# Kernel optimization log

Hardware: AMD Instinct MI355X
Metric: run time of the kernel (lower is better)

The kernel has to match this reference:

```python
import jax, jax.numpy as jnp
import numpy as np

DIM = 1024
D_STATE = 16
D_CONV = 4
EXPAND = 2
D_INNER = EXPAND * DIM          # 2048
DT_RANK = (DIM + 15) // 16      # 64 (math.ceil(d_model/16))
BSZ = 2
SEQ = 2048


def setup_inputs() -> dict:
    key = jax.random.key(0)
    ks = jax.random.split(key, 8)
    g = lambda k, shape, scale: (jax.random.normal(k, shape, jnp.float32) * scale)
    return {
        "x": g(ks[0], (BSZ, SEQ, DIM), 1.0),
        # in_proj: Linear(d_model -> 2*d_inner, bias=False)
        "W_in": g(ks[1], (2 * D_INNER, DIM), DIM ** -0.5),
        # depthwise causal conv1d: groups=d_inner, kernel d_conv, bias=True
        "conv_w": g(ks[2], (D_INNER, 1, D_CONV), D_CONV ** -0.5),
        "conv_b": jnp.zeros((D_INNER,), jnp.float32),
        # x_proj: Linear(d_inner -> dt_rank + 2*d_state, bias=False)
        "W_xproj": g(ks[3], (DT_RANK + 2 * D_STATE, D_INNER), D_INNER ** -0.5),
        # dt_proj: Linear(dt_rank -> d_inner, bias=True)
        "W_dt": g(ks[4], (D_INNER, DT_RANK), DT_RANK ** -0.5),
        "b_dt": g(ks[5], (D_INNER,), 0.1),
        # S4D-real init: A = -exp(A_log), A_log = log(1..d_state)
        "A_log": jnp.log(jnp.broadcast_to(
            jnp.arange(1, D_STATE + 1, dtype=jnp.float32), (D_INNER, D_STATE))),
        "D": jnp.ones((D_INNER,), jnp.float32),
        # out_proj: Linear(d_inner -> d_model, bias=False)
        "W_out": g(ks[6], (DIM, D_INNER), D_INNER ** -0.5),
        # wrapper LayerNorm(dim)
        "gamma": jnp.ones((DIM,), jnp.float32),
        "beta": jnp.zeros((DIM,), jnp.float32),
    }


def reference(x, W_in, conv_w, conv_b, W_xproj, W_dt, b_dt,
              A_log, D, W_out, gamma, beta):
    B, L, _ = x.shape
    # ---- input projection, split into conv path and gate ----
    xz = x @ W_in.T                              # (B, L, 2*d_inner)
    xc, z = jnp.split(xz, 2, axis=-1)
    # ---- depthwise causal conv1d + SiLU ----
    xt = jnp.transpose(xc, (0, 2, 1))            # (B, d_inner, L)
    conv = jax.lax.conv_general_dilated(
        xt, conv_w, window_strides=(1,), padding=[(D_CONV - 1, 0)],
        dimension_numbers=("NCH", "OIH", "NCH"), feature_group_count=D_INNER)
    u = jax.nn.silu(jnp.transpose(conv + conv_b[None, :, None], (0, 2, 1)))  # (B,L,d_inner)
    # ---- input-dependent delta, B, C ----
    xdbc = u @ W_xproj.T                          # (B, L, dt_rank + 2*d_state)
    dt = xdbc[..., :DT_RANK]
    Bm = xdbc[..., DT_RANK:DT_RANK + D_STATE]     # (B, L, d_state)
    Cm = xdbc[..., DT_RANK + D_STATE:]            # (B, L, d_state)
    delta = jax.nn.softplus(dt @ W_dt.T + b_dt)   # (B, L, d_inner)
    A = -jnp.exp(A_log)                           # (d_inner, d_state)
    # ---- selective scan: h_t = exp(dt*A) h_{t-1} + dt*B_t*u_t ; y_t = <h_t, C_t> ----
    def step(h, inputs):
        d_t, u_t, B_t, C_t = inputs               # (B,d_inner),(B,d_inner),(B,S),(B,S)
        dA = jnp.exp(d_t[:, :, None] * A)         # (B, d_inner, S)
        h = h * dA + (d_t * u_t)[:, :, None] * B_t[:, None, :]
        y = jnp.einsum("bds,bs->bd", h, C_t)
        return h, y
    tm = lambda a: jnp.transpose(a, (1, 0, 2))    # time-major for scan
    h0 = jnp.zeros((B, D_INNER, D_STATE), x.dtype)
    _, ys = jax.lax.scan(step, h0, (tm(delta), tm(u), tm(Bm), tm(Cm)))
    y = jnp.transpose(ys, (1, 0, 2)) + u * D      # skip term D*u
    y = y * jax.nn.silu(z)                        # gate
    out = y @ W_out.T                             # (B, L, dim)
    # ---- wrapper LayerNorm(dim), eps=1e-5 ----
    mean = out.mean(-1, keepdims=True)
    var = out.var(-1, keepdims=True)
    return (out - mean) * jax.lax.rsqrt(var + 1e-5) * gamma + beta
```

## Files before the change

### kernel.cpp

```cpp
#include <hip/hip_runtime.h>
#include <stdint.h>

typedef unsigned short u16;
typedef __bf16 bf16x8 __attribute__((ext_vector_type(8)));
typedef unsigned short u16x8 __attribute__((ext_vector_type(8)));
typedef unsigned short u16x4 __attribute__((ext_vector_type(4)));
typedef float f32x4 __attribute__((ext_vector_type(4)));

#define BSZ 2
#define SEQ 2048
#define DIM 1024
#define D_INNER 2048
#define DT_RANK 64
#define D_STATE 16
#define XPROJ_N 96
#define NCHUNK 32
#define CHUNK_T 64
#define LOG2E 1.44269504f

#define N_X   4194304
#define N_W   4194304
#define N_WX  196608
#define N_WDT 131072
#define N_WO  2097152
#define N_XD  393216

__device__ __forceinline__ float bf2f(u16 h) {
    return __uint_as_float(((unsigned)h) << 16);
}
__device__ __forceinline__ u16 f2bf(float f) {
    unsigned u = __float_as_uint(f);
    unsigned r = (u + 0x7FFFu + ((u >> 16) & 1u)) >> 16;
    return (u16)r;
}

__device__ __forceinline__ f32x4 mfma16(bf16x8 a, bf16x8 b, f32x4 c) {
    return __builtin_amdgcn_mfma_f32_16x16x32_bf16(a, b, c, 0, 0, 0);
}

__device__ __forceinline__ void gload_lds16(const void* g, void* l) {
    __builtin_amdgcn_global_load_lds(
        (const __attribute__((address_space(1))) unsigned int*)(uintptr_t)g,
        (__attribute__((address_space(3))) unsigned int*)(uintptr_t)l,
        16, 0, 0);
}

__device__ __forceinline__ void split4(const float* __restrict__ in,
                                       u16* __restrict__ hi, u16* __restrict__ lo,
                                       long i)
{
    f32x4 v = *(const f32x4*)(in + i);
    u16x4 h, l;
    #pragma unroll
    for (int j = 0; j < 4; j++) {
        u16 hh = f2bf(v[j]);
        h[j] = hh;
        l[j] = f2bf(v[j] - bf2f(hh));
    }
    *(u16x4*)(hi + i) = h;
    *(u16x4*)(lo + i) = l;
}

__global__ __launch_bounds__(256)
void megasplit4(const float* __restrict__ x,  u16* __restrict__ xh,  u16* __restrict__ xl,
                const float* __restrict__ w,  u16* __restrict__ wh,  u16* __restrict__ wl,
                const float* __restrict__ wx, u16* __restrict__ wxh, u16* __restrict__ wxl,
                const float* __restrict__ wd, u16* __restrict__ wdh, u16* __restrict__ wdl)
{
    long i = ((long)blockIdx.x * 256 + threadIdx.x) * 4;
    if (i < N_X) { split4(x, xh, xl, i); return; }
    i -= N_X;
    if (i < N_W) { split4(w, wh, wl, i); return; }
    i -= N_W;
    if (i < N_WX) { split4(wx, wxh, wxl, i); return; }
    i -= N_WX;
    if (i < N_WDT) { split4(wd, wdh, wdl, i); }
}

enum { EPI_XZ = 0, EPI_F32 = 1, EPI_SOFTPLUS = 2 };

template<int TERMS, int EPI>
__global__ __launch_bounds__(256)
void gemm128(const u16* __restrict__ Ah, const u16* __restrict__ Al, int lda,
             const u16* __restrict__ Bh, const u16* __restrict__ Bl, int ldb,
             void* __restrict__ C, void* __restrict__ C2, int ldc,
             int K, const float* __restrict__ bias)
{
    __shared__ u16 lds[(TERMS == 3) ? 16384 : 12288];
    u16* Ah_l = lds;
    u16* Al_l = lds + 4096;
    u16* Bh_l = lds + ((TERMS == 3) ? 8192 : 4096);
    u16* Bl_l = lds + ((TERMS == 3) ? 12288 : 8192);

    const int tid  = threadIdx.x;
    const int w    = tid >> 6;
    const int lane = tid & 63;
    const int r16  = lane & 15;
    const int quad = lane >> 4;
    const int wr   = w >> 1;
    const int wc   = w & 1;
    const long m0  = (long)blockIdx.y * 128;
    const long n0  = (long)blockIdx.x * 128;

    const int c0 = w * 64 + lane;
    const int c1 = 256 + c0;
    const int ma0 = c0 >> 2, kca0 = ((c0 & 3) ^ ((ma0 >> 1) & 3)) * 8;
    const int ma1 = c1 >> 2, kca1 = ((c1 & 3) ^ ((ma1 >> 1) & 3)) * 8;

    const u16* Arow0 = Ah + (m0 + ma0) * (long)lda + kca0;
    const u16* Arow1 = Ah + (m0 + ma1) * (long)lda + kca1;
    const u16* Alrow0 = (TERMS == 3) ? Al + (m0 + ma0) * (long)lda + kca0 : nullptr;
    const u16* Alrow1 = (TERMS == 3) ? Al + (m0 + ma1) * (long)lda + kca1 : nullptr;
    const u16* Brow0 = Bh + (n0 + ma0) * (long)ldb + kca0;
    const u16* Brow1 = Bh + (n0 + ma1) * (long)ldb + kca1;
    const u16* Blrow0 = Bl + (n0 + ma0) * (long)ldb + kca0;
    const u16* Blrow1 = Bl + (n0 + ma1) * (long)ldb + kca1;

    f32x4 acc[4][4];
    #pragma unroll
    for (int i = 0; i < 4; i++)
        #pragma unroll
        for (int j = 0; j < 4; j++) acc[i][j] = {0.f, 0.f, 0.f, 0.f};

    int caof[4], cbof[4];
    #pragma unroll
    for (int i = 0; i < 4; i++) {
        int m = wr * 64 + i * 16 + r16;
        caof[i] = (m * 4 + (quad ^ ((m >> 1) & 3))) * 8;
        int n = wc * 64 + i * 16 + r16;
        cbof[i] = (n * 4 + (quad ^ ((n >> 1) & 3))) * 8;
    }

    for (int k0 = 0; k0 < K; k0 += 32) {
        __syncthreads();
        gload_lds16(Arow0 + k0, Ah_l + c0 * 8);
        gload_lds16(Arow1 + k0, Ah_l + c1 * 8);
        if (TERMS == 3) {
            gload_lds16(Alrow0 + k0, Al_l + c0 * 8);
            gload_lds16(Alrow1 + k0, Al_l + c1 * 8);
        }
        gload_lds16(Brow0 + k0, Bh_l + c0 * 8);
        gload_lds16(Brow1 + k0, Bh_l + c1 * 8);
        gload_lds16(Blrow0 + k0, Bl_l + c0 * 8);
        gload_lds16(Blrow1 + k0, Bl_l + c1 * 8);
        __syncthreads();

        bf16x8 fah[4], fal[4], fbh[4], fbl[4];
        #pragma unroll
        for (int i = 0; i < 4; i++) {
            fah[i] = *(const bf16x8*)(Ah_l + caof[i]);
            if (TERMS == 3) fal[i] = *(const bf16x8*)(Al_l + caof[i]);
            fbh[i] = *(const bf16x8*)(Bh_l + cbof[i]);
            fbl[i] = *(const bf16x8*)(Bl_l + cbof[i]);
        }
        #pragma unroll
        for (int i = 0; i < 4; i++) {
            #pragma unroll
            for (int j = 0; j < 4; j++) {
                acc[i][j] = mfma16(fah[i], fbh[j], acc[i][j]);
                acc[i][j] = mfma16(fah[i], fbl[j], acc[i][j]);
                if (TERMS == 3) acc[i][j] = mfma16(fal[i], fbh[j], acc[i][j]);
            }
        }
    }

    #pragma unroll
    for (int i = 0; i < 4; i++) {
        #pragma unroll
        for (int j = 0; j < 4; j++) {
            long col = n0 + wc * 64 + j * 16 + r16;
            #pragma unroll
            for (int r = 0; r < 4; r++) {
                long row = m0 + wr * 64 + i * 16 + quad * 4 + r;
                float x = acc[i][j][r];
                if (EPI == EPI_XZ) {
                    if (col < D_INNER) ((u16*)C)[row * (long)D_INNER + col] = f2bf(x);
                    else ((float*)C2)[row * (long)D_INNER + (col - D_INNER)] = x;
                } else if (EPI == EPI_SOFTPLUS) {
                    x += bias[col];
                    x = (x > 15.f) ? x : log1pf(__expf(x));
                    ((float*)C)[row * (long)ldc + col] = x;
                } else {
                    ((float*)C)[row * (long)ldc + col] = x;
                }
            }
        }
    }
}

__global__ __launch_bounds__(256)
void gemm128_sk2(const u16* __restrict__ Ah, int lda,
                 const u16* __restrict__ Bh, const u16* __restrict__ Bl, int ldb,
                 float* __restrict__ OutBase, int ldc, int K0)
{
    __shared__ u16 lds[12288];
    u16* Ah_l = lds;
    u16* Bh_l = lds + 4096;
    u16* Bl_l = lds + 8192;

    const int tid  = threadIdx.x;
    const int w    = tid >> 6;
    const int lane = tid & 63;
    const int r16  = lane & 15;
    const int quad = lane >> 4;
    const int wr   = w >> 1;
    const int wc   = w & 1;
    const long m0  = (long)blockIdx.y * 128;
    const long n0  = (long)blockIdx.x * 128;
    const int kbase = blockIdx.z * K0;
    float* Out = OutBase + (long)blockIdx.z * 4194304;

    const int c0 = w * 64 + lane;
    const int c1 = 256 + c0;
    const int ma0 = c0 >> 2, kca0 = ((c0 & 3) ^ ((ma0 >> 1) & 3)) * 8;
    const int ma1 = c1 >> 2, kca1 = ((c1 & 3) ^ ((ma1 >> 1) & 3)) * 8;

    const u16* Arow0 = Ah + (m0 + ma0) * (long)lda + kbase + kca0;
    const u16* Arow1 = Ah + (m0 + ma1) * (long)lda + kbase + kca1;
    const u16* Brow0 = Bh + (n0 + ma0) * (long)ldb + kbase + kca0;
    const u16* Brow1 = Bh + (n0 + ma1) * (long)ldb + kbase + kca1;
    const u16* Blrow0 = Bl + (n0 + ma0) * (long)ldb + kbase + kca0;
    const u16* Blrow1 = Bl + (n0 + ma1) * (long)ldb + kbase + kca1;

    f32x4 acc[4][4];
    #pragma unroll
    for (int i = 0; i < 4; i++)
        #pragma unroll
        for (int j = 0; j < 4; j++) acc[i][j] = {0.f, 0.f, 0.f, 0.f};

    int caof[4], cbof[4];
    #pragma unroll
    for (int i = 0; i < 4; i++) {
        int m = wr * 64 + i * 16 + r16;
        caof[i] = (m * 4 + (quad ^ ((m >> 1) & 3))) * 8;
        int n = wc * 64 + i * 16 + r16;
        cbof[i] = (n * 4 + (quad ^ ((n >> 1) & 3))) * 8;
    }

    for (int k0 = 0; k0 < K0; k0 += 32) {
        __syncthreads();
        gload_lds16(Arow0 + k0, Ah_l + c0 * 8);
        gload_lds16(Arow1 + k0, Ah_l + c1 * 8);
        gload_lds16(Brow0 + k0, Bh_l + c0 * 8);
        gload_lds16(Brow1 + k0, Bh_l + c1 * 8);
        gload_lds16(Blrow0 + k0, Bl_l + c0 * 8);
        gload_lds16(Blrow1 + k0, Bl_l + c1 * 8);
        __syncthreads();

        bf16x8 fah[4], fbh[4], fbl[4];
        #pragma unroll
        for (int i = 0; i < 4; i++) {
            fah[i] = *(const bf16x8*)(Ah_l + caof[i]);
            fbh[i] = *(const bf16x8*)(Bh_l + cbof[i]);
            fbl[i] = *(const bf16x8*)(Bl_l + cbof[i]);
        }
        #pragma unroll
        for (int i = 0; i < 4; i++) {
            #pragma unroll
            for (int j = 0; j < 4; j++) {
                acc[i][j] = mfma16(fah[i], fbh[j], acc[i][j]);
                acc[i][j] = mfma16(fah[i], fbl[j], acc[i][j]);
            }
        }
    }

    #pragma unroll
    for (int i = 0; i < 4; i++) {
        #pragma unroll
        for (int j = 0; j < 4; j++) {
            long col = n0 + wc * 64 + j * 16 + r16;
            #pragma unroll
            for (int r = 0; r < 4; r++) {
                long row = m0 + wr * 64 + i * 16 + quad * 4 + r;
                Out[row * (long)ldc + col] = acc[i][j][r];
            }
        }
    }
}

__global__ __launch_bounds__(64)
void gemm_dt32(const u16* __restrict__ Ah, const u16* __restrict__ Al, int lda,
               const u16* __restrict__ Bh, const u16* __restrict__ Bl, int ldb,
               float* __restrict__ C, int ldc, const float* __restrict__ bias)
{
    const int lane = threadIdx.x;
    const int r16  = lane & 15;
    const int quad = lane >> 4;
    const long m0 = (long)blockIdx.y * 32;
    const long n0 = (long)blockIdx.x * 32;

    const u16* Ah0 = Ah + (m0 + r16) * (long)lda + quad * 8;
    const u16* Ah1 = Ah0 + 16L * lda;
    const u16* Al0 = Al + (m0 + r16) * (long)lda + quad * 8;
    const u16* Al1 = Al0 + 16L * lda;
    const u16* Bh0 = Bh + (n0 + r16) * (long)ldb + quad * 8;
    const u16* Bh1 = Bh0 + 16L * ldb;
    const u16* Bl0 = Bl + (n0 + r16) * (long)ldb + quad * 8;
    const u16* Bl1 = Bl0 + 16L * ldb;

    f32x4 acc00 = {0,0,0,0}, acc01 = {0,0,0,0}, acc10 = {0,0,0,0}, acc11 = {0,0,0,0};

    #pragma unroll
    for (int k = 0; k < DT_RANK; k += 32) {
        bf16x8 a0h = *(const bf16x8*)(Ah0 + k);
        bf16x8 a1h = *(const bf16x8*)(Ah1 + k);
        bf16x8 a0l = *(const bf16x8*)(Al0 + k);
        bf16x8 a1l = *(const bf16x8*)(Al1 + k);
        bf16x8 b0h = *(const bf16x8*)(Bh0 + k);
        bf16x8 b1h = *(const bf16x8*)(Bh1 + k);
        bf16x8 b0l = *(const bf16x8*)(Bl0 + k);
        bf16x8 b1l = *(const bf16x8*)(Bl1 + k);
        acc00 = mfma16(a0h, b0h, acc00); acc00 = mfma16(a0h, b0l, acc00); acc00 = mfma16(a0l, b0h, acc00);
        acc01 = mfma16(a0h, b1h, acc01); acc01 = mfma16(a0h, b1l, acc01); acc01 = mfma16(a0l, b1h, acc01);
        acc10 = mfma16(a1h, b0h, acc10); acc10 = mfma16(a1h, b0l, acc10); acc10 = mfma16(a1l, b0h, acc10);
        acc11 = mfma16(a1h, b1h, acc11); acc11 = mfma16(a1h, b1l, acc11); acc11 = mfma16(a1l, b1h, acc11);
    }

    #pragma unroll
    for (int i = 0; i < 2; i++) {
        #pragma unroll
        for (int j = 0; j < 2; j++) {
            f32x4 v = (i == 0) ? (j == 0 ? acc00 : acc01) : (j == 0 ? acc10 : acc11);
            long col = n0 + j * 16 + r16;
            #pragma unroll
            for (int r = 0; r < 4; r++) {
                long row = m0 + i * 16 + quad * 4 + r;
                float x = v[r] + bias[col];
                x = (x > 15.f) ? x : log1pf(__expf(x));
                C[row * (long)ldc + col] = x;
            }
        }
    }
}

__global__ __launch_bounds__(64)
void gemm3_skp(const u16* __restrict__ A, int lda,
               const u16* __restrict__ Bh, const u16* __restrict__ Bl, int ldb,
               float* __restrict__ Cpart, int ldc, int K0)
{
    const int lane = threadIdx.x;
    const int r16  = lane & 15;
    const int quad = lane >> 4;
    const long m0 = (long)blockIdx.y * 32;
    const long n0 = (long)blockIdx.x * 32;
    const int kbase = blockIdx.z * K0;
    float* C = Cpart + (long)blockIdx.z * N_XD;

    const u16* Ap0 = A  + (m0 + r16) * (long)lda + quad * 8 + kbase;
    const u16* Ap1 = Ap0 + 16L * lda;
    const u16* Bh0 = Bh + (n0 + r16) * (long)ldb + quad * 8 + kbase;
    const u16* Bh1 = Bh0 + 16L * ldb;
    const u16* Bl0 = Bl + (n0 + r16) * (long)ldb + quad * 8 + kbase;
    const u16* Bl1 = Bl0 + 16L * ldb;

    f32x4 acc00 = {0,0,0,0}, acc01 = {0,0,0,0}, acc10 = {0,0,0,0}, acc11 = {0,0,0,0};

    for (int k = 0; k < K0; k += 32) {
        bf16x8 a0 = *(const bf16x8*)(Ap0 + k);
        bf16x8 a1 = *(const bf16x8*)(Ap1 + k);
        bf16x8 b0h = *(const bf16x8*)(Bh0 + k);
        bf16x8 b1h = *(const bf16x8*)(Bh1 + k);
        bf16x8 b0l = *(const bf16x8*)(Bl0 + k);
        bf16x8 b1l = *(const bf16x8*)(Bl1 + k);
        acc00 = mfma16(a0, b0h, acc00); acc00 = mfma16(a0, b0l, acc00);
        acc01 = mfma16(a0, b1h, acc01); acc01 = mfma16(a0, b1l, acc01);
        acc10 = mfma16(a1, b0h, acc10); acc10 = mfma16(a1, b0l, acc10);
        acc11 = mfma16(a1, b1h, acc11); acc11 = mfma16(a1, b1l, acc11);
    }

    #pragma unroll
    for (int i = 0; i < 2; i++) {
        #pragma unroll
        for (int j = 0; j < 2; j++) {
            f32x4 v = (i == 0) ? (j == 0 ? acc00 : acc01) : (j == 0 ? acc10 : acc11);
            long col = n0 + j * 16 + r16;
            #pragma unroll
            for (int r = 0; r < 4; r++) {
                long row = m0 + i * 16 + quad * 4 + r;
                C[row * (long)ldc + col] = v[r];
            }
        }
    }
}

__global__ __launch_bounds__(256)
void combine3(const float* __restrict__ part, float* __restrict__ xdbc,
              u16* __restrict__ hi, u16* __restrict__ lo)
{
    long i = ((long)blockIdx.x * 256 + threadIdx.x) * 4;
    if (i >= N_XD) return;
    f32x4 s = *(const f32x4*)(part + i);
    #pragma unroll
    for (int j = 1; j < 8; j++) {
        f32x4 p = *(const f32x4*)(part + (long)j * N_XD + i);
        s[0] += p[0]; s[1] += p[1]; s[2] += p[2]; s[3] += p[3];
    }
    *(f32x4*)(xdbc + i) = s;
    u16x4 h, l;
    #pragma unroll
    for (int j = 0; j < 4; j++) {
        u16 hh = f2bf(s[j]);
        h[j] = hh;
        l[j] = f2bf(s[j] - bf2f(hh));
    }
    *(u16x4*)(hi + i) = h;
    *(u16x4*)(lo + i) = l;
}

__global__ __launch_bounds__(256)
void conv_silu(const u16* __restrict__ xc, const float* __restrict__ cw,
               const float* __restrict__ cb, u16* __restrict__ u)
{
    long idx = ((long)blockIdx.x * 256 + threadIdx.x) * 8;
    int t  = (int)((idx >> 11) & 2047);
    int d0 = (int)(idx & 2047);

    bf16x8 xrow[4];
    #pragma unroll
    for (int j = 0; j < 4; j++) {
        int tt = t - 3 + j;
        if (tt >= 0) xrow[j] = *(const bf16x8*)(xc + idx + (long)(j - 3) * D_INNER);
        else         xrow[j] = bf16x8{0,0,0,0,0,0,0,0};
    }
    u16x8 out;
    #pragma unroll
    for (int e = 0; e < 8; e++) {
        int d = d0 + e;
        float acc = cb[d];
        #pragma unroll
        for (int j = 0; j < 4; j++)
            acc += cw[d * 4 + j] * (float)xrow[j][e];
        out[e] = f2bf(acc / (1.f + __expf(-acc)));
    }
    *(u16x8*)(u + idx) = out;
}

__global__ __launch_bounds__(256)
void scan_partA(const float* __restrict__ delta, const u16* __restrict__ u,
                const float* __restrict__ xdbc, const float* __restrict__ A_log,
                float* __restrict__ hbuf, float* __restrict__ sdelta,
                const float* __restrict__ wout, u16* __restrict__ wouth,
                u16* __restrict__ woutl)
{
    const int d = blockIdx.x * 256 + threadIdx.x;
    const int c = blockIdx.y;
    const int b = blockIdx.z;
    const int t0 = c * CHUNK_T;

    float Af[16];
    #pragma unroll
    for (int s = 0; s < 16; s++) Af[s] = -__expf(A_log[d * 16 + s]) * LOG2E;

    float h[16];
    #pragma unroll
    for (int s = 0; s < 16; s++) h[s] = 0.f;
    float sd = 0.f;

    const float* dptr = delta + ((long)b * SEQ + t0) * D_INNER + d;
    const u16*   uptr = u     + ((long)b * SEQ + t0) * D_INNER + d;
    const float* xp   = xdbc  + ((long)b * SEQ + t0) * XPROJ_N;

    for (int t = 0; t < CHUNK_T; t++) {
        float dl = dptr[(long)t * D_INNER];
        float uu = bf2f(uptr[(long)t * D_INNER]);
        f32x4 B0 = *(const f32x4*)(xp + t * XPROJ_N + DT_RANK);
        f32x4 B1 = *(const f32x4*)(xp + t * XPROJ_N + DT_RANK + 4);
        f32x4 B2 = *(const f32x4*)(xp + t * XPROJ_N + DT_RANK + 8);
        f32x4 B3 = *(const f32x4*)(xp + t * XPROJ_N + DT_RANK + 12);
        float Bv[16] = {B0[0],B0[1],B0[2],B0[3], B1[0],B1[1],B1[2],B1[3],
                        B2[0],B2[1],B2[2],B2[3], B3[0],B3[1],B3[2],B3[3]};
        sd += dl;
        float dlu = dl * uu;
        #pragma unroll
        for (int s = 0; s < 16; s++)
            h[s] = h[s] * exp2f(dl * Af[s]) + dlu * Bv[s];
    }

    float* hout = hbuf + ((long)(b * NCHUNK + c) * D_INNER + d) * 16;
    #pragma unroll
    for (int s = 0; s < 16; s++) hout[s] = h[s];
    sdelta[(long)(b * NCHUNK + c) * D_INNER + d] = sd;

    long tidg = (((long)b * NCHUNK + c) * 8 + blockIdx.x) * 256 + threadIdx.x;
    long base = tidg * 16;
    #pragma unroll
    for (int k = 0; k < 4; k++) split4(wout, wouth, woutl, base + 4 * k);
}

__global__ __launch_bounds__(256)
void scan_fixup(float* __restrict__ hbuf, const float* __restrict__ sdelta,
                const float* __restrict__ A_log)
{
    const int idx = blockIdx.x * 256 + threadIdx.x;
    const int ds = idx & (D_INNER * 16 - 1);
    const int b  = idx >> 15;
    const float Af = -__expf(A_log[ds]) * LOG2E;
    float hin = 0.f;
    #pragma unroll 4
    for (int c = 0; c < NCHUNK; c++) {
        long gi = (long)(b * NCHUNK + c) * (D_INNER * 16) + ds;
        float e = hbuf[gi];
        hbuf[gi] = hin;
        float sd = sdelta[(long)(b * NCHUNK + c) * D_INNER + (ds >> 4)];
        hin = e + exp2f(Af * sd) * hin;
    }
}

__global__ __launch_bounds__(256)
void scan_partC(const float* __restrict__ delta, const u16* __restrict__ u,
                const float* __restrict__ xdbc, const float* __restrict__ z,
                const float* __restrict__ A_log, const float* __restrict__ Dp,
                const float* __restrict__ hbuf, u16* __restrict__ y)
{
    const int d = blockIdx.x * 256 + threadIdx.x;
    const int c = blockIdx.y;
    const int b = blockIdx.z;
    const int t0 = c * CHUNK_T;

    float Af[16];
    #pragma unroll
    for (int s = 0; s < 16; s++) Af[s] = -__expf(A_log[d * 16 + s]) * LOG2E;
    const float Dd = Dp[d];

    float h[16];
    const float* hin = hbuf + ((long)(b * NCHUNK + c) * D_INNER + d) * 16;
    #pragma unroll
    for (int s = 0; s < 16; s++) h[s] = hin[s];

    const float* dptr = delta + ((long)b * SEQ + t0) * D_INNER + d;
    const u16*   uptr = u     + ((long)b * SEQ + t0) * D_INNER + d;
    const float* zptr = z     + ((long)b * SEQ + t0) * D_INNER + d;
    const float* xp   = xdbc  + ((long)b * SEQ + t0) * XPROJ_N;
    u16* yptr = y + ((long)b * SEQ + t0) * D_INNER + d;

    for (int t = 0; t < CHUNK_T; t++) {
        float dl = dptr[(long)t * D_INNER];
        float uu = bf2f(uptr[(long)t * D_INNER]);
        float zl = zptr[(long)t * D_INNER];
        f32x4 B0 = *(const f32x4*)(xp + t * XPROJ_N + DT_RANK);
        f32x4 B1 = *(const f32x4*)(xp + t * XPROJ_N + DT_RANK + 4);
        f32x4 B2 = *(const f32x4*)(xp + t * XPROJ_N + DT_RANK + 8);
        f32x4 B3 = *(const f32x4*)(xp + t * XPROJ_N + DT_RANK + 12);
        f32x4 C0 = *(const f32x4*)(xp + t * XPROJ_N + DT_RANK + 16);
        f32x4 C1 = *(const f32x4*)(xp + t * XPROJ_N + DT_RANK + 20);
        f32x4 C2 = *(const f32x4*)(xp + t * XPROJ_N + DT_RANK + 24);
        f32x4 C3 = *(const f32x4*)(xp + t * XPROJ_N + DT_RANK + 28);
        float Bv[16] = {B0[0],B0[1],B0[2],B0[3], B1[0],B1[1],B1[2],B1[3],
                        B2[0],B2[1],B2[2],B2[3], B3[0],B3[1],B3[2],B3[3]};
        float Cv[16] = {C0[0],C0[1],C0[2],C0[3], C1[0],C1[1],C1[2],C1[3],
                        C2[0],C2[1],C2[2],C2[3], C3[0],C3[1],C3[2],C3[3]};
        float dlu = dl * uu;
        float p0 = 0.f, p1 = 0.f, p2 = 0.f, p3 = 0.f;
        #pragma unroll
        for (int s = 0; s < 16; s += 4) {
            h[s]   = h[s]   * exp2f(dl * Af[s])   + dlu * Bv[s];
            h[s+1] = h[s+1] * exp2f(dl * Af[s+1]) + dlu * Bv[s+1];
            h[s+2] = h[s+2] * exp2f(dl * Af[s+2]) + dlu * Bv[s+2];
            h[s+3] = h[s+3] * exp2f(dl * Af[s+3]) + dlu * Bv[s+3];
            p0 += h[s]   * Cv[s];
            p1 += h[s+1] * Cv[s+1];
            p2 += h[s+2] * Cv[s+2];
            p3 += h[s+3] * Cv[s+3];
        }
        float acc = (p0 + p1) + (p2 + p3);
        float sz = zl / (1.f + __expf(-zl));
        float yy = (acc + uu * Dd) * sz;
        yptr[(long)t * D_INNER] = f2bf(yy);
    }
}

__global__ __launch_bounds__(256)
void layernorm_kernel(const float* __restrict__ pa, const float* __restrict__ pb,
                      const float* __restrict__ gamma, const float* __restrict__ beta,
                      float* __restrict__ out)
{
    const long row = blockIdx.x;
    const long base = row * DIM;
    int tid = threadIdx.x;
    float v[4];
    float sum = 0.f, sq = 0.f;
    #pragma unroll
    for (int i = 0; i < 4; i++) {
        long c = base + tid + i * 256;
        v[i] = pa[c] + pb[c];
        sum += v[i];
        sq  += v[i] * v[i];
    }
    #pragma unroll
    for (int off = 1; off < 64; off <<= 1) {
        sum += __shfl_xor(sum, off);
        sq  += __shfl_xor(sq, off);
    }
    __shared__ float ssum[4], ssq[4];
    int w = tid >> 6;
    if ((tid & 63) == 0) { ssum[w] = sum; ssq[w] = sq; }
    __syncthreads();
    float ts = ssum[0] + ssum[1] + ssum[2] + ssum[3];
    float tq = ssq[0] + ssq[1] + ssq[2] + ssq[3];
    float mean = ts * (1.f / DIM);
    float var  = tq * (1.f / DIM) - mean * mean;
    float rstd = rsqrtf(var + 1e-5f);
    float* o = out + base;
    #pragma unroll
    for (int i = 0; i < 4; i++) {
        int c = tid + i * 256;
        o[c] = (v[i] - mean) * rstd * gamma[c] + beta[c];
    }
}

extern "C" void kernel_launch(void* const* d_in, const int* in_sizes, int n_in,
                              void* d_out, int out_size, void* d_ws, size_t ws_size,
                              hipStream_t stream)
{
    const float* x      = (const float*)d_in[0];
    const float* W_in   = (const float*)d_in[1];
    const float* conv_w = (const float*)d_in[2];
    const float* conv_b = (const float*)d_in[3];
    const float* W_xproj= (const float*)d_in[4];
    const float* W_dt   = (const float*)d_in[5];
    const float* b_dt   = (const float*)d_in[6];
    const float* A_log  = (const float*)d_in[7];
    const float* Dv     = (const float*)d_in[8];
    const float* W_out  = (const float*)d_in[9];
    const float* gamma  = (const float*)d_in[10];
    const float* beta   = (const float*)d_in[11];

    char* ws = (char*)d_ws;
    u16*   xc    = (u16*)(ws);
    float* g3p   = (float*)(ws);
    u16*   xdh   = (u16*)(ws + 12582912);
    u16*   xdl   = (u16*)(ws + 14155776);
    float* hbuf  = (float*)(ws);
    u16*   wouth = (u16*)(ws + 8388608);
    u16*   woutl = (u16*)(ws + 12582912);
    float* z     = (float*)(ws + 16777216);
    float* opre  = (float*)(ws + 16777216);
    u16*   u     = (u16*)(ws + 50331648);
    u16*   xh    = (u16*)(ws + 67108864);
    u16*   xl    = (u16*)(ws + 75497472);
    u16*   wh    = (u16*)(ws + 83886080);
    u16*   wl    = (u16*)(ws + 92274688);
    float* delta = (float*)(ws + 67108864);
    float* xdbc  = (float*)(ws + 100663296);
    u16*   wxh   = (u16*)(ws + 102236160);
    u16*   wxl   = (u16*)(ws + 102629376);
    u16*   wdth  = (u16*)(ws + 103022592);
    u16*   wdtl  = (u16*)(ws + 103284736);
    float* sdel  = (float*)(ws + 103546880);
    u16*   yb    = (u16*)d_out;

    megasplit4<<<8512, 256, 0, stream>>>(x, xh, xl, W_in, wh, wl,
                                         W_xproj, wxh, wxl, W_dt, wdth, wdtl);
    gemm128<3, EPI_XZ><<<dim3(32, 32), 256, 0, stream>>>(
        xh, xl, DIM, wh, wl, DIM, xc, z, 0, DIM, nullptr);
    conv_silu<<<4096, 256, 0, stream>>>(xc, conv_w, conv_b, u);
    gemm3_skp<<<dim3(3, 128, 8), 64, 0, stream>>>(
        u, D_INNER, wxh, wxl, D_INNER, g3p, XPROJ_N, 256);
    combine3<<<384, 256, 0, stream>>>(g3p, xdbc, xdh, xdl);
    gemm_dt32<<<dim3(64, 128), 64, 0, stream>>>(
        xdh, xdl, XPROJ_N, wdth, wdtl, DT_RANK, delta, D_INNER, b_dt);
    scan_partA<<<dim3(8, NCHUNK, BSZ), 256, 0, stream>>>(
        delta, u, xdbc, A_log, hbuf, sdel, W_out, wouth, woutl);
    scan_fixup<<<256, 256, 0, stream>>>(hbuf, sdel, A_log);
    scan_partC<<<dim3(8, NCHUNK, BSZ), 256, 0, stream>>>(delta, u, xdbc, z, A_log, Dv, hbuf, yb);
    gemm128_sk2<<<dim3(8, 32, 2), 256, 0, stream>>>(
        yb, D_INNER, wouth, woutl, D_INNER, opre, DIM, 1024);
    layernorm_kernel<<<4096, 256, 0, stream>>>(
        opre, opre + 4194304, gamma, beta, (float*)d_out);
}
```

Before: 457.7 us.

## Replace in_proj GEMM with 256x256 triple-buffered pipelined kernel over split terms

The generic 128x128 three-term bf16 GEMM for the input projection is replaced by a dedicated 512-thread kernel with 256x256 tiles. The hi/lo split terms are serialized as three passes over K (96 k-steps), with a three-stage LDS ring buffer, async loads issued two steps ahead, and s_setprio around the MFMA blocks. The aim is to raise data reuse per tile, hide global-load latency behind MFMA work, and drop a sync per step. In exchange it uses much more LDS and registers, and the grid shrinks to 256 blocks, which may leave compute units underused.

```diff
diff --git a/kernel.cpp b/kernel.cpp
--- a/kernel.cpp
+++ b/kernel.cpp
@@ -77,112 +77,120 @@
     if (i < N_WDT) { split4(wd, wdh, wdl, i); }
 }
 
-enum { EPI_XZ = 0, EPI_F32 = 1, EPI_SOFTPLUS = 2 };
-
-template<int TERMS, int EPI>
-__global__ __launch_bounds__(256)
-void gemm128(const u16* __restrict__ Ah, const u16* __restrict__ Al, int lda,
-             const u16* __restrict__ Bh, const u16* __restrict__ Bl, int ldb,
-             void* __restrict__ C, void* __restrict__ C2, int ldc,
-             int K, const float* __restrict__ bias)
-{
-    __shared__ u16 lds[(TERMS == 3) ? 16384 : 12288];
-    u16* Ah_l = lds;
-    u16* Al_l = lds + 4096;
-    u16* Bh_l = lds + ((TERMS == 3) ? 8192 : 4096);
-    u16* Bl_l = lds + ((TERMS == 3) ? 12288 : 8192);
+__global__ __launch_bounds__(512, 2)
+void gemm256_xz(const u16* __restrict__ xh, const u16* __restrict__ xl,
+                const u16* __restrict__ wh, const u16* __restrict__ wl,
+                u16* __restrict__ xc, float* __restrict__ z)
+{
+    __shared__ u16 lds[49152];
 
     const int tid  = threadIdx.x;
     const int w    = tid >> 6;
     const int lane = tid & 63;
     const int r16  = lane & 15;
     const int quad = lane >> 4;
-    const int wr   = w >> 1;
-    const int wc   = w & 1;
-    const long m0  = (long)blockIdx.y * 128;
-    const long n0  = (long)blockIdx.x * 128;
-
-    const int c0 = w * 64 + lane;
-    const int c1 = 256 + c0;
-    const int ma0 = c0 >> 2, kca0 = ((c0 & 3) ^ ((ma0 >> 1) & 3)) * 8;
-    const int ma1 = c1 >> 2, kca1 = ((c1 & 3) ^ ((ma1 >> 1) & 3)) * 8;
-
-    const u16* Arow0 = Ah + (m0 + ma0) * (long)lda + kca0;
-    const u16* Arow1 = Ah + (m0 + ma1) * (long)lda + kca1;
-    const u16* Alrow0 = (TERMS == 3) ? Al + (m0 + ma0) * (long)lda + kca0 : nullptr;
-    const u16* Alrow1 = (TERMS == 3) ? Al + (m0 + ma1) * (long)lda + kca1 : nullptr;
-    const u16* Brow0 = Bh + (n0 + ma0) * (long)ldb + kca0;
-    const u16* Brow1 = Bh + (n0 + ma1) * (long)ldb + kca1;
-    const u16* Blrow0 = Bl + (n0 + ma0) * (long)ldb + kca0;
-    const u16* Blrow1 = Bl + (n0 + ma1) * (long)ldb + kca1;
-
-    f32x4 acc[4][4];
-    #pragma unroll
-    for (int i = 0; i < 4; i++)
+    const int wr   = w >> 2;
+    const int wc   = w & 3;
+    const long m0  = (long)blockIdx.y * 256;
+    const long n0  = (long)blockIdx.x * 256;
+
+    const int c0 = tid, c1 = tid + 512;
+    const int ma0 = c0 >> 2, kc0 = ((c0 & 3) ^ ((ma0 >> 1) & 3)) * 8;
+    const int ma1 = c1 >> 2, kc1 = ((c1 & 3) ^ ((ma1 >> 1) & 3)) * 8;
+    const int arow0 = ((int)m0 + ma0) * DIM + kc0;
+    const int arow1 = ((int)m0 + ma1) * DIM + kc1;
+    const int brow0 = ((int)n0 + ma0) * DIM + kc0;
+    const int brow1 = ((int)n0 + ma1) * DIM + kc1;
+
+    int caof[8], cbof[4];
+    #pragma unroll
+    for (int i = 0; i < 8; i++) {
+        int m = wr * 128 + i * 16 + r16;
+        caof[i] = (m * 4 + (quad ^ ((m >> 1) & 3))) * 8;
+    }
+    #pragma unroll
+    for (int j = 0; j < 4; j++) {
+        int n = wc * 64 + j * 16 + r16;
+        cbof[j] = (n * 4 + (quad ^ ((n >> 1) & 3))) * 8;
+    }
+
+    f32x4 acc[8][4];
+    #pragma unroll
+    for (int i = 0; i < 8; i++)
         #pragma unroll
         for (int j = 0; j < 4; j++) acc[i][j] = {0.f, 0.f, 0.f, 0.f};
 
-    int caof[4], cbof[4];
-    #pragma unroll
-    for (int i = 0; i < 4; i++) {
-        int m = wr * 64 + i * 16 + r16;
-        caof[i] = (m * 4 + (quad ^ ((m >> 1) & 3))) * 8;
-        int n = wc * 64 + i * 16 + r16;
-        cbof[i] = (n * 4 + (quad ^ ((n >> 1) & 3))) * 8;
-    }
-
-    for (int k0 = 0; k0 < K; k0 += 32) {
-        __syncthreads();
-        gload_lds16(Arow0 + k0, Ah_l + c0 * 8);
-        gload_lds16(Arow1 + k0, Ah_l + c1 * 8);
-        if (TERMS == 3) {
-            gload_lds16(Alrow0 + k0, Al_l + c0 * 8);
-            gload_lds16(Alrow1 + k0, Al_l + c1 * 8);
-        }
-        gload_lds16(Brow0 + k0, Bh_l + c0 * 8);
-        gload_lds16(Brow1 + k0, Bh_l + c1 * 8);
-        gload_lds16(Blrow0 + k0, Bl_l + c0 * 8);
-        gload_lds16(Blrow1 + k0, Bl_l + c1 * 8);
-        __syncthreads();
-
-        bf16x8 fah[4], fal[4], fbh[4], fbl[4];
-        #pragma unroll
-        for (int i = 0; i < 4; i++) {
-            fah[i] = *(const bf16x8*)(Ah_l + caof[i]);
-            if (TERMS == 3) fal[i] = *(const bf16x8*)(Al_l + caof[i]);
-            fbh[i] = *(const bf16x8*)(Bh_l + cbof[i]);
-            fbl[i] = *(const bf16x8*)(Bl_l + cbof[i]);
-        }
-        #pragma unroll
-        for (int i = 0; i < 4; i++) {
-            #pragma unroll
-            for (int j = 0; j < 4; j++) {
-                acc[i][j] = mfma16(fah[i], fbh[j], acc[i][j]);
-                acc[i][j] = mfma16(fah[i], fbl[j], acc[i][j]);
-                if (TERMS == 3) acc[i][j] = mfma16(fal[i], fbh[j], acc[i][j]);
-            }
-        }
-    }
-
-    #pragma unroll
-    for (int i = 0; i < 4; i++) {
+    gload_lds16(xh + arow0,      lds + c0 * 8);
+    gload_lds16(xh + arow1,      lds + c1 * 8);
+    gload_lds16(wh + brow0,      lds + 24576 + c0 * 8);
+    gload_lds16(wh + brow1,      lds + 24576 + c1 * 8);
+    gload_lds16(xh + arow0 + 32, lds + 8192 + c0 * 8);
+    gload_lds16(xh + arow1 + 32, lds + 8192 + c1 * 8);
+    gload_lds16(wh + brow0 + 32, lds + 24576 + 8192 + c0 * 8);
+    gload_lds16(wh + brow1 + 32, lds + 24576 + 8192 + c1 * 8);
+    asm volatile("s_waitcnt vmcnt(4)" ::: "memory");
+    __builtin_amdgcn_s_barrier();
+
+    int kt = 0;
+#define XZ_ITER(CUR, SL)                                                      \
+  {                                                                           \
+    int st = kt + 2; if (st > 95) st = 95;                                    \
+    const int ts = st >> 5;                                                   \
+    const int kb = (st & 31) * 32;                                            \
+    const u16* As = (ts < 2) ? xh : xl;                                       \
+    const u16* Bs = (ts == 1) ? wl : wh;                                      \
+    const u16* Alds = lds + (CUR) * 8192;                                     \
+    const u16* Blds = lds + 24576 + (CUR) * 8192;                             \
+                     \
+    gload_lds16(As + arow0 + kb, lds + (SL) * 8192 + c0 * 8);                 \
+    gload_lds16(As + arow1 + kb, lds + (SL) * 8192 + c1 * 8);                 \
+    bf16x8 bfr[4], afr[4];                                                    \
+    _Pragma("unroll") for (int j = 0; j < 4; j++)                             \
+        bfr[j] = *(const bf16x8*)(Blds + cbof[j]);                            \
+    _Pragma("unroll") for (int i = 0; i < 4; i++)                             \
+        afr[i] = *(const bf16x8*)(Alds + caof[i]);                            \
+    __builtin_amdgcn_s_setprio(1);                                            \
+    _Pragma("unroll") for (int i = 0; i < 4; i++)                             \
+      _Pragma("unroll") for (int j = 0; j < 4; j++)                           \
+        acc[i][j] = mfma16(afr[i], bfr[j], acc[i][j]);                        \
+    __builtin_amdgcn_s_setprio(0);                                            \
+                             \
+    gload_lds16(Bs + brow0 + kb, lds + 24576 + (SL) * 8192 + c0 * 8);         \
+    gload_lds16(Bs + brow1 + kb, lds + 24576 + (SL) * 8192 + c1 * 8);         \
+    bf16x8 af2[4];                                                            \
+    _Pragma("unroll") for (int i = 0; i < 4; i++)                             \
+        af2[i] = *(const bf16x8*)(Alds + caof[4 + i]);                        \
+    __builtin_amdgcn_s_setprio(1);                                            \
+    _Pragma("unroll") for (int i = 0; i < 4; i++)                             \
+      _Pragma("unroll") for (int j = 0; j < 4; j++)                           \
+        acc[4 + i][j] = mfma16(af2[i], bfr[j], acc[4 + i][j]);                \
+    __builtin_amdgcn_s_setprio(0);                                            \
+    asm volatile("s_waitcnt vmcnt(4)" ::: "memory");                          \
+    __builtin_amdgcn_s_barrier();                                             \
+    kt++;                                                                     \
+  }
+
+    #pragma unroll 1
+    for (int it = 0; it < 32; it++) {
+        XZ_ITER(0, 2)
+        XZ_ITER(1, 0)
+        XZ_ITER(2, 1)
+    }
+#undef XZ_ITER
+
+    asm volatile("s_waitcnt vmcnt(0)" ::: "memory");
+
+    const bool isz = (n0 >= 2048);
+    #pragma unroll
+    for (int i = 0; i < 8; i++) {
         #pragma unroll
         for (int j = 0; j < 4; j++) {
             long col = n0 + wc * 64 + j * 16 + r16;
             #pragma unroll
             for (int r = 0; r < 4; r++) {
-                long row = m0 + wr * 64 + i * 16 + quad * 4 + r;
-                float x = acc[i][j][r];
-                if (EPI == EPI_XZ) {
-                    if (col < D_INNER) ((u16*)C)[row * (long)D_INNER + col] = f2bf(x);
-                    else ((float*)C2)[row * (long)D_INNER + (col - D_INNER)] = x;
-                } else if (EPI == EPI_SOFTPLUS) {
-                    x += bias[col];
-                    x = (x > 15.f) ? x : log1pf(__expf(x));
-                    ((float*)C)[row * (long)ldc + col] = x;
-                } else {
-                    ((float*)C)[row * (long)ldc + col] = x;
-                }
+                long row = m0 + wr * 128 + i * 16 + quad * 4 + r;
+                if (!isz) xc[row * (long)D_INNER + col] = f2bf(acc[i][j][r]);
+                else      z[row * (long)D_INNER + (col - D_INNER)] = acc[i][j][r];
             }
         }
     }
@@ -651,8 +659,7 @@
 
     megasplit4<<<8512, 256, 0, stream>>>(x, xh, xl, W_in, wh, wl,
                                          W_xproj, wxh, wxl, W_dt, wdth, wdtl);
-    gemm128<3, EPI_XZ><<<dim3(32, 32), 256, 0, stream>>>(
-        xh, xl, DIM, wh, wl, DIM, xc, z, 0, DIM, nullptr);
+    gemm256_xz<<<dim3(16, 16), 512, 0, stream>>>(xh, xl, wh, wl, xc, z);
     conv_silu<<<4096, 256, 0, stream>>>(xc, conv_w, conv_b, u);
     gemm3_skp<<<dim3(3, 128, 8), 64, 0, stream>>>(
         u, D_INNER, wxh, wxl, D_INNER, g3p, XPROJ_N, 256);
```

Measured after the change: 441.9 us. -3.4%, faster.
